# Optimization experiments

Measured on AMD Instinct MI355X. Metric: run time of the kernel, lower is better.

The kernel has to match this reference:

```python
import jax, jax.numpy as jnp
import numpy as np

B, N, P, D = 32, 8, 6, 96
E, H, I, K, NL = 128, 8, 64, 32, 2
L = N * D  # transformer sequence length = 768
OUT = 128
EPS = 1e-5


def _layernorm(x, s, b):
    m = jnp.mean(x, axis=-1, keepdims=True)
    v = jnp.mean((x - m) ** 2, axis=-1, keepdims=True)
    return (x - m) / jnp.sqrt(v + EPS) * s + b


def _pos_encoding(length, d_model):
    pos = jnp.arange(length, dtype=jnp.float32)[:, None]
    div = jnp.exp(jnp.arange(0, d_model, 2, dtype=jnp.float32) * (-jnp.log(10000.0) / d_model))
    ang = pos * div  # [L, E/2]
    return jnp.stack([jnp.sin(ang), jnp.cos(ang)], axis=-1).reshape(length, d_model)


def setup_inputs() -> dict:
    key = jax.random.key(0)
    ks = jax.random.split(key, 20)
    s = 0.02
    return {
        "x": jax.random.normal(ks[0], (B, N, P, D), jnp.float32),
        "prototypes": jax.random.normal(ks[1], (D, K, P), jnp.float32),
        "emb_w": jax.random.normal(ks[2], (E, P), jnp.float32) * s,
        "emb_b": jnp.zeros((E,), jnp.float32),
        "proj_w": jax.random.normal(ks[3], (E, P), jnp.float32) * s,
        "proj_b": jnp.zeros((E,), jnp.float32),
        "in_proj_w": jax.random.normal(ks[4], (NL, 3 * E, E), jnp.float32) * s,
        "in_proj_b": jnp.zeros((NL, 3 * E), jnp.float32),
        "out_proj_w": jax.random.normal(ks[5], (NL, E, E), jnp.float32) * s,
        "out_proj_b": jnp.zeros((NL, E), jnp.float32),
        "ln1_s": jnp.ones((NL, E), jnp.float32),
        "ln1_b": jnp.zeros((NL, E), jnp.float32),
        "ffn_w1": jax.random.normal(ks[6], (NL, I, E), jnp.float32) * s,
        "ffn_b1": jnp.zeros((NL, I), jnp.float32),
        "ffn_w2": jax.random.normal(ks[7], (NL, E, I), jnp.float32) * s,
        "ffn_b2": jnp.zeros((NL, E), jnp.float32),
        "ln2_s": jnp.ones((NL, E), jnp.float32),
        "ln2_b": jnp.zeros((NL, E), jnp.float32),
        "out_w": jax.random.normal(ks[8], (OUT, L * E), jnp.float32) * s,
        "out_b": jnp.zeros((OUT,), jnp.float32),
    }


def reference(x, prototypes, emb_w, emb_b, proj_w, proj_b,
              in_proj_w, in_proj_b, out_proj_w, out_proj_b,
              ln1_s, ln1_b, ffn_w1, ffn_b1, ffn_w2, ffn_b2,
              ln2_s, ln2_b, out_w, out_b):
    # Faithful to torch .view: raw row-major reinterpretation [B,N,P,D] -> [B*N*D, P]
    x_flat = x.reshape(B * N * D, P)
    x_normed = x_flat / jnp.maximum(jnp.linalg.norm(x_flat, axis=1, keepdims=True), 1e-12)
    x_norm = x_normed.reshape(B, N, D, P)
    p_normed = prototypes / jnp.maximum(jnp.linalg.norm(prototypes, axis=2, keepdims=True), 1e-12)

    # Vectorized per-dim cosine-sim argmax + gather (replaces the Python loop over D)
    sim = jnp.einsum('bndp,dkp->bndk', x_norm, p_normed)  # [B,N,D,K]
    best_idx = jnp.argmax(sim, axis=3)                    # [B,N,D]
    d_idx = jnp.arange(D)[None, None, :]
    selected = p_normed[d_idx, best_idx]                  # [B,N,D,P]

    input_embed = (x_flat @ emb_w.T + emb_b).reshape(B, N, D, E)
    proto_embed = (selected.reshape(B * N * D, P) @ proj_w.T + proj_b).reshape(B, N, D, E)
    seq = (input_embed + proto_embed).reshape(B, L, E)
    seq = seq + _pos_encoding(L, E)[None]

    scale = 1.0 / jnp.sqrt(jnp.float32(E // H))
    for l in range(NL):
        qkv = seq @ in_proj_w[l].T + in_proj_b[l]          # [B,L,3E]
        q, k, v = jnp.split(qkv, 3, axis=-1)
        q = q.reshape(B, L, H, E // H)
        k = k.reshape(B, L, H, E // H)
        v = v.reshape(B, L, H, E // H)
        logits = jnp.einsum('blhd,bmhd->bhlm', q, k) * scale
        attn = jax.nn.softmax(logits, axis=-1)
        ctx = jnp.einsum('bhlm,bmhd->blhd', attn, v).reshape(B, L, E)
        attn_out = ctx @ out_proj_w[l].T + out_proj_b[l]
        seq = _layernorm(seq + attn_out, ln1_s[l], ln1_b[l])
        h = jax.nn.elu(seq @ ffn_w1[l].T + ffn_b1[l])
        ffn_out = h @ ffn_w2[l].T + ffn_b2[l]
        seq = _layernorm(seq + ffn_out, ln2_s[l], ln2_b[l])

    z = seq.reshape(B, L * E)
    return z @ out_w.T + out_b
```

## Files before the change

### kernel.cpp

```cpp
#include <hip/hip_runtime.h>
#include <hip/hip_bf16.h>
#include <math.h>

typedef unsigned short ushort_t;
typedef unsigned int uint_t;

#define BB 32
#define PP 6
#define DD 96
#define EE 128
#define HH 8
#define II 64
#define KK 32
#define LSEQ 768
#define ROWS (BB * LSEQ)
#define OUTN 128
#define KOUT (LSEQ * EE)

using bf16x8 = __attribute__((ext_vector_type(8))) short;
using bf16x4 = __attribute__((ext_vector_type(4))) short;
using f32x4  = __attribute__((ext_vector_type(4))) float;
using u32x4  = __attribute__((ext_vector_type(4))) uint_t;

__device__ __forceinline__ ushort_t f2b(float f) {
    __hip_bfloat16 h = __float2bfloat16(f);
    return *reinterpret_cast<ushort_t*>(&h);
}
__device__ __forceinline__ uint_t permpack(float hi, float lo) {
    return __builtin_amdgcn_perm(__builtin_bit_cast(uint_t, hi),
                                 __builtin_bit_cast(uint_t, lo), 0x07060302u);
}

__global__ void cast_all_kernel(
    const float* __restrict__ s0, int n0, const float* __restrict__ s1, int n1,
    const float* __restrict__ s2, int n2, const float* __restrict__ s3, int n3,
    ushort_t* __restrict__ d0, ushort_t* __restrict__ d1,
    ushort_t* __restrict__ d2, ushort_t* __restrict__ d3,
    float* __restrict__ peT)
{
    int i = blockIdx.x * 256 + threadIdx.x;
    if (i < n0) { d0[i] = f2b(s0[i]); return; }
    i -= n0;
    if (i < n1) { d1[i] = f2b(s1[i]); return; }
    i -= n1;
    if (i < n2) { d2[i] = f2b(s2[i]); return; }
    i -= n2;
    if (i < n3) { d3[i] = f2b(s3[i]); return; }
    i -= n3;
    const int lpos = i >> 7, tt = i & 127;
    const float twoj = (float)((tt >> 1) * 2);
    const float div = __expf(twoj * (-9.210340371976184f / 128.0f));
    const float ang = (float)lpos * div;
    peT[i] = (tt & 1) ? __cosf(ang) : __sinf(ang);
}

__global__ __launch_bounds__(128) void embed_kernel(
    const float* __restrict__ x, const float* __restrict__ prot,
    const float* __restrict__ emb_w, const float* __restrict__ emb_b,
    const float* __restrict__ proj_w, const float* __restrict__ proj_b,
    const float* __restrict__ peT,
    float* __restrict__ seq, ushort_t* __restrict__ seq_bf)
{
    const int r = blockIdx.x;
    const int t = threadIdx.x;
    __shared__ float xrow[PP];
    __shared__ float sel[PP];

    if (t < PP) xrow[t] = x[r * PP + t];
    __syncthreads();

    float nx = 0.f;
    #pragma unroll
    for (int p = 0; p < PP; ++p) nx += xrow[p] * xrow[p];
    const float xinv = 1.f / fmaxf(sqrtf(nx), 1e-12f);

    const int d = r % DD;
    if (t < KK) {
        const float* pr = prot + (d * KK + t) * PP;
        float pp[PP];
        float np2 = 0.f;
        #pragma unroll
        for (int p = 0; p < PP; ++p) { pp[p] = pr[p]; np2 += pp[p] * pp[p]; }
        const float pinv = 1.f / fmaxf(sqrtf(np2), 1e-12f);
        float dot = 0.f;
        #pragma unroll
        for (int p = 0; p < PP; ++p) dot += xrow[p] * pp[p];
        float sim = dot * xinv * pinv;
        int k = t;
        #pragma unroll
        for (int off = 16; off; off >>= 1) {
            float osim = __shfl_down(sim, off);
            int   ok   = __shfl_down(k, off);
            if (osim > sim || (osim == sim && ok < k)) { sim = osim; k = ok; }
        }
        k = __shfl(k, 0);
        if (t == k) {
            #pragma unroll
            for (int p = 0; p < PP; ++p) sel[p] = pp[p] * pinv;
        }
    }
    __syncthreads();

    float acc = emb_b[t] + proj_b[t];
    #pragma unroll
    for (int p = 0; p < PP; ++p) acc = fmaf(xrow[p], emb_w[t * PP + p], acc);
    #pragma unroll
    for (int p = 0; p < PP; ++p) acc = fmaf(sel[p], proj_w[t * PP + p], acc);

    const int lpos = r % LSEQ;
    const float v = acc + peT[lpos * EE + t];
    seq[(size_t)r * EE + t] = v;
    seq_bf[(size_t)r * EE + t] = f2b(v);
}

__global__ __launch_bounds__(256) void gemm_qkv(
    const ushort_t* __restrict__ A, const ushort_t* __restrict__ W,
    const float* __restrict__ bias,
    ushort_t* __restrict__ q_bf, ushort_t* __restrict__ k2,
    ushort_t* __restrict__ v2)
{
    __shared__ ushort_t Ws[64 * 136];
    const int t = threadIdx.x;
    const int wave = t >> 6, lane = t & 63;
    const int quad = lane >> 4, l16 = lane & 15;
    const int m0 = blockIdx.y * 128, n0 = blockIdx.x * 64;

    for (int c = t; c < 64 * 16; c += 256) {
        int row = c >> 4, col = c & 15;
        *(bf16x8*)&Ws[row * 136 + col * 8] =
            *(const bf16x8*)&W[(size_t)(n0 + row) * 128 + col * 8];
    }
    __syncthreads();

    f32x4 acc[2][4];
    #pragma unroll
    for (int s = 0; s < 2; ++s)
        #pragma unroll
        for (int nt = 0; nt < 4; ++nt)
            acc[s][nt] = (f32x4){0.f, 0.f, 0.f, 0.f};

    const ushort_t* a0p = A + (size_t)(m0 + wave * 32 + l16) * 128 + quad * 8;
    const ushort_t* a1p = a0p + (size_t)16 * 128;
    const ushort_t* wp  = &Ws[l16 * 136 + quad * 8];

    #pragma unroll
    for (int k0 = 0; k0 < 128; k0 += 32) {
        bf16x8 a0 = *(const bf16x8*)(a0p + k0);
        bf16x8 a1 = *(const bf16x8*)(a1p + k0);
        #pragma unroll
        for (int nt = 0; nt < 4; ++nt) {
            bf16x8 wf = *(const bf16x8*)(wp + nt * 16 * 136 + k0);
            acc[0][nt] = __builtin_amdgcn_mfma_f32_16x16x32_bf16(wf, a0, acc[0][nt], 0, 0, 0);
            acc[1][nt] = __builtin_amdgcn_mfma_f32_16x16x32_bf16(wf, a1, acc[1][nt], 0, 0, 0);
        }
    }

    const int b = blockIdx.y / 6;
    #pragma unroll
    for (int s = 0; s < 2; ++s) {
        const int m = m0 + wave * 32 + s * 16 + l16;
        const int l = m - b * LSEQ;
        const int c4 = l >> 4, r16 = l & 15;
        #pragma unroll
        for (int nt = 0; nt < 4; ++nt) {
            const int nb = n0 + nt * 16 + quad * 4;
            float4 b4 = *(const float4*)&bias[nb];
            float v[4];
            #pragma unroll
            for (int r = 0; r < 4; ++r)
                v[r] = acc[s][nt][r] + ((const float*)&b4)[r];

            if (n0 < 128) {
                #pragma unroll
                for (int r = 0; r < 4; ++r) v[r] *= 0.36067376022224085f;
                uint2 w2;
                w2.x = permpack(v[1], v[0]);
                w2.y = permpack(v[3], v[2]);
                *(uint2*)&q_bf[(size_t)m * EE + nb] = w2;
            } else if (n0 < 256) {
                const int h = ((n0 - 128) >> 4) + nt;
                uint2 w2;
                w2.x = permpack(v[1], v[0]);
                w2.y = permpack(v[3], v[2]);
                *(uint2*)&k2[((((size_t)(b * HH + h)) * 48 + c4) * 4 + quad) * 64 + r16 * 4] = w2;
            } else {
                const int h = ((n0 - 256) >> 4) + nt;
                const size_t vbase = (((size_t)(b * HH + h)) * 48 + c4) * 16;
                #pragma unroll
                for (int r = 0; r < 4; ++r)
                    v2[(vbase + quad * 4 + r) * 16 + r16] = f2b(v[r]);
            }
        }
    }
}

__global__ __launch_bounds__(256) void attention_mfma(
    const ushort_t* __restrict__ q_bf, const ushort_t* __restrict__ k2,
    const ushort_t* __restrict__ v2, ushort_t* __restrict__ ctx)
{
    const int bh = blockIdx.x;
    const int b = bh & 31, h = bh >> 5;
    const int qb = blockIdx.y;
    const int t = threadIdx.x;
    const int wave = t >> 6, lane = t & 63;
    const int quad = lane >> 4, l16 = lane & 15;
    const int hoff = h * 16;

    bf16x4 qf[2];
    #pragma unroll
    for (int s = 0; s < 2; ++s) {
        int row = b * LSEQ + qb * 128 + wave * 32 + s * 16 + l16;
        qf[s] = *(const bf16x4*)&q_bf[(size_t)row * EE + hoff + quad * 4];
    }

    const int bhn = b * HH + h;
    const ushort_t* kp = k2 + (size_t)bhn * 12288 + quad * 64 + l16 * 4;
    const ushort_t* vp = v2 + (size_t)bhn * 12288 + l16 * 16 + quad * 4;

    f32x4 oacc[2], lacc[2];
    oacc[0] = (f32x4){0.f, 0.f, 0.f, 0.f};
    oacc[1] = (f32x4){0.f, 0.f, 0.f, 0.f};
    lacc[0] = (f32x4){0.f, 0.f, 0.f, 0.f};
    lacc[1] = (f32x4){0.f, 0.f, 0.f, 0.f};
    const f32x4 zero4 = (f32x4){0.f, 0.f, 0.f, 0.f};
    bf16x4 ones4;
    #pragma unroll
    for (int j = 0; j < 4; ++j) ones4[j] = (short)0x3F80;

    bf16x4 kA = *(const bf16x4*)(kp);
    bf16x4 vA = *(const bf16x4*)(vp);
    bf16x4 kB = *(const bf16x4*)(kp + 256);
    bf16x4 vB = *(const bf16x4*)(vp + 256);

    for (int c4 = 0; c4 < 48; ++c4) {
        const int c4n = c4 < 46 ? c4 + 2 : 0;
        bf16x4 kC = *(const bf16x4*)(kp + c4n * 256);
        bf16x4 vC = *(const bf16x4*)(vp + c4n * 256);

        #pragma unroll
        for (int s = 0; s < 2; ++s) {
            f32x4 sv = __builtin_amdgcn_mfma_f32_16x16x16bf16_1k(kA, qf[s], zero4, 0, 0, 0);
            float e0 = __builtin_amdgcn_exp2f(sv[0]);
            float e1 = __builtin_amdgcn_exp2f(sv[1]);
            float e2 = __builtin_amdgcn_exp2f(sv[2]);
            float e3 = __builtin_amdgcn_exp2f(sv[3]);
            uint2 pu;
            pu.x = permpack(e1, e0);
            pu.y = permpack(e3, e2);
            bf16x4 pf = __builtin_bit_cast(bf16x4, pu);
            oacc[s] = __builtin_amdgcn_mfma_f32_16x16x16bf16_1k(vA, pf, oacc[s], 0, 0, 0);
            lacc[s] = __builtin_amdgcn_mfma_f32_16x16x16bf16_1k(ones4, pf, lacc[s], 0, 0, 0);
        }
        kA = kB; vA = vB; kB = kC; vB = vC;
    }

    #pragma unroll
    for (int s = 0; s < 2; ++s) {
        const float inv = 1.f / lacc[s][0];
        const int q = qb * 128 + wave * 32 + s * 16 + l16;
        uint2 w2;
        w2.x = permpack(oacc[s][1] * inv, oacc[s][0] * inv);
        w2.y = permpack(oacc[s][3] * inv, oacc[s][2] * inv);
        *(uint2*)&ctx[((size_t)(b * LSEQ + q)) * EE + hoff + quad * 4] = w2;
    }
}

__global__ __launch_bounds__(256) void gemm_ln_direct(
    const ushort_t* __restrict__ A, const ushort_t* __restrict__ W,
    const float* __restrict__ bias,
    const float* __restrict__ gamma, const float* __restrict__ beta,
    float* __restrict__ seq, ushort_t* __restrict__ seq_bf, int K)
{
    __shared__ ushort_t Ws[128 * 136];
    const int t = threadIdx.x;
    const int wave = t >> 6, lane = t & 63;
    const int quad = lane >> 4, l16 = lane & 15;
    const int m0 = blockIdx.x * 64;
    const int kp = K + 8;
    const int ak8 = K >> 3;

    for (int c = t; c < 128 * ak8; c += 256) {
        int row = c / ak8, col = c - row * ak8;
        *(bf16x8*)&Ws[row * kp + col * 8] =
            *(const bf16x8*)&W[(size_t)row * K + col * 8];
    }
    __syncthreads();

    f32x4 acc[8];
    #pragma unroll
    for (int nt = 0; nt < 8; ++nt) acc[nt] = (f32x4){0.f, 0.f, 0.f, 0.f};

    const int m = m0 + wave * 16 + l16;
    const ushort_t* ap = A + (size_t)m * K + quad * 8;
    const ushort_t* wp = &Ws[l16 * kp + quad * 8];

    for (int k0 = 0; k0 < K; k0 += 32) {
        bf16x8 a = *(const bf16x8*)(ap + k0);
        #pragma unroll
        for (int nt = 0; nt < 8; ++nt) {
            bf16x8 wf = *(const bf16x8*)(wp + nt * 16 * kp + k0);
            acc[nt] = __builtin_amdgcn_mfma_f32_16x16x32_bf16(wf, a, acc[nt], 0, 0, 0);
        }
    }

    float v[8][4];
    float s = 0.f;
    #pragma unroll
    for (int nt = 0; nt < 8; ++nt) {
        const int nb = nt * 16 + quad * 4;
        float4 b4 = *(const float4*)&bias[nb];
        float4 r4 = *(const float4*)&seq[(size_t)m * EE + nb];
        #pragma unroll
        for (int r = 0; r < 4; ++r) {
            v[nt][r] = acc[nt][r] + ((const float*)&b4)[r] + ((const float*)&r4)[r];
            s += v[nt][r];
        }
    }
    s += __shfl_xor(s, 16);
    s += __shfl_xor(s, 32);
    const float mean = s * (1.f / 128.f);
    float s2 = 0.f;
    #pragma unroll
    for (int nt = 0; nt < 8; ++nt)
        #pragma unroll
        for (int r = 0; r < 4; ++r) {
            float d = v[nt][r] - mean;
            s2 += d * d;
        }
    s2 += __shfl_xor(s2, 16);
    s2 += __shfl_xor(s2, 32);
    const float rstd = 1.f / sqrtf(s2 * (1.f / 128.f) + 1e-5f);

    #pragma unroll
    for (int nt = 0; nt < 8; ++nt) {
        const int nb = nt * 16 + quad * 4;
        float4 g4 = *(const float4*)&gamma[nb];
        float4 be4 = *(const float4*)&beta[nb];
        float y[4];
        #pragma unroll
        for (int r = 0; r < 4; ++r)
            y[r] = (v[nt][r] - mean) * rstd * ((const float*)&g4)[r] + ((const float*)&be4)[r];
        float4 f4 = {y[0], y[1], y[2], y[3]};
        *(float4*)&seq[(size_t)m * EE + nb] = f4;
        uint2 w2;
        w2.x = permpack(y[1], y[0]);
        w2.y = permpack(y[3], y[2]);
        *(uint2*)&seq_bf[(size_t)m * EE + nb] = w2;
    }
}

__global__ __launch_bounds__(256) void ffn_fused(
    const ushort_t* __restrict__ seq_bf_in, const ushort_t* __restrict__ W1,
    const float* __restrict__ b1, const ushort_t* __restrict__ W2,
    const float* __restrict__ b2,
    const float* __restrict__ gamma, const float* __restrict__ beta,
    float* __restrict__ seq, ushort_t* __restrict__ seq_bf)
{
    __shared__ ushort_t W1s[64 * 136];
    __shared__ ushort_t W2s[128 * 72];
    __shared__ ushort_t Hs[64 * 72];
    const int t = threadIdx.x;
    const int wave = t >> 6, lane = t & 63;
    const int quad = lane >> 4, l16 = lane & 15;
    const int m0 = blockIdx.x * 64;

    for (int c = t; c < 64 * 16; c += 256) {
        int row = c >> 4, col = c & 15;
        *(bf16x8*)&W1s[row * 136 + col * 8] =
            *(const bf16x8*)&W1[(size_t)row * 128 + col * 8];
    }
    for (int c = t; c < 128 * 8; c += 256) {
        int row = c >> 3, col = c & 7;
        *(bf16x8*)&W2s[row * 72 + col * 8] =
            *(const bf16x8*)&W2[(size_t)row * 64 + col * 8];
    }
    __syncthreads();

    const int lrow = wave * 16 + l16;
    const int m = m0 + lrow;
    f32x4 acc1[4];
    #pragma unroll
    for (int nt = 0; nt < 4; ++nt) acc1[nt] = (f32x4){0.f, 0.f, 0.f, 0.f};

    const ushort_t* ap = seq_bf_in + (size_t)m * EE + quad * 8;
    const ushort_t* w1p = &W1s[l16 * 136 + quad * 8];
    for (int k0 = 0; k0 < 128; k0 += 32) {
        bf16x8 a = *(const bf16x8*)(ap + k0);
        #pragma unroll
        for (int nt = 0; nt < 4; ++nt) {
            bf16x8 wf = *(const bf16x8*)(w1p + nt * 16 * 136 + k0);
            acc1[nt] = __builtin_amdgcn_mfma_f32_16x16x32_bf16(wf, a, acc1[nt], 0, 0, 0);
        }
    }
    #pragma unroll
    for (int nt = 0; nt < 4; ++nt) {
        const int ib = nt * 16 + quad * 4;
        float4 b4 = *(const float4*)&b1[ib];
        float hv[4];
        #pragma unroll
        for (int r = 0; r < 4; ++r) {
            float u = acc1[nt][r] + ((const float*)&b4)[r];
            hv[r] = u > 0.f ? u : expm1f(u);
        }
        uint2 w2;
        w2.x = permpack(hv[1], hv[0]);
        w2.y = permpack(hv[3], hv[2]);
        *(uint2*)&Hs[lrow * 72 + ib] = w2;
    }

    f32x4 acc2[8];
    #pragma unroll
    for (int nt = 0; nt < 8; ++nt) acc2[nt] = (f32x4){0.f, 0.f, 0.f, 0.f};
    const ushort_t* hp = &Hs[lrow * 72 + quad * 8];
    const ushort_t* w2p = &W2s[l16 * 72 + quad * 8];
    #pragma unroll
    for (int k0 = 0; k0 < 64; k0 += 32) {
        bf16x8 hf = *(const bf16x8*)(hp + k0);
        #pragma unroll
        for (int nt = 0; nt < 8; ++nt) {
            bf16x8 wf = *(const bf16x8*)(w2p + nt * 16 * 72 + k0);
            acc2[nt] = __builtin_amdgcn_mfma_f32_16x16x32_bf16(wf, hf, acc2[nt], 0, 0, 0);
        }
    }

    float v[8][4];
    float s = 0.f;
    #pragma unroll
    for (int nt = 0; nt < 8; ++nt) {
        const int nb = nt * 16 + quad * 4;
        float4 b4 = *(const float4*)&b2[nb];
        float4 r4 = *(const float4*)&seq[(size_t)m * EE + nb];
        #pragma unroll
        for (int r = 0; r < 4; ++r) {
            v[nt][r] = acc2[nt][r] + ((const float*)&b4)[r] + ((const float*)&r4)[r];
            s += v[nt][r];
        }
    }
    s += __shfl_xor(s, 16);
    s += __shfl_xor(s, 32);
    const float mean = s * (1.f / 128.f);
    float s2 = 0.f;
    #pragma unroll
    for (int nt = 0; nt < 8; ++nt)
        #pragma unroll
        for (int r = 0; r < 4; ++r) {
            float d = v[nt][r] - mean;
            s2 += d * d;
        }
    s2 += __shfl_xor(s2, 16);
    s2 += __shfl_xor(s2, 32);
    const float rstd = 1.f / sqrtf(s2 * (1.f / 128.f) + 1e-5f);

    #pragma unroll
    for (int nt = 0; nt < 8; ++nt) {
        const int nb = nt * 16 + quad * 4;
        float4 g4 = *(const float4*)&gamma[nb];
        float4 be4 = *(const float4*)&beta[nb];
        float y[4];
        #pragma unroll
        for (int r = 0; r < 4; ++r)
            y[r] = (v[nt][r] - mean) * rstd * ((const float*)&g4)[r] + ((const float*)&be4)[r];
        float4 f4 = {y[0], y[1], y[2], y[3]};
        *(float4*)&seq[(size_t)m * EE + nb] = f4;
        uint2 w2;
        w2.x = permpack(y[1], y[0]);
        w2.y = permpack(y[3], y[2]);
        *(uint2*)&seq_bf[(size_t)m * EE + nb] = w2;
    }
}

#define PKC 192
#define PNBLK (KOUT / PKC)
__global__ __launch_bounds__(256) void out_gemm3(
    const ushort_t* __restrict__ seqbf, const float* __restrict__ out_w,
    float* __restrict__ part)
{
    const int t = threadIdx.x;
    const int wave = t >> 6, lane = t & 63;
    const int quad = lane >> 4, l16 = lane & 15;
    const size_t k0 = (size_t)blockIdx.x * PKC;
    const int n0 = wave * 32;

    f32x4 acc[2][2];
    #pragma unroll
    for (int mt = 0; mt < 2; ++mt)
        #pragma unroll
        for (int nt = 0; nt < 2; ++nt)
            acc[mt][nt] = (f32x4){0.f, 0.f, 0.f, 0.f};

    const ushort_t* a0p = seqbf + (size_t)l16 * KOUT + k0 + quad * 8;
    const ushort_t* a1p = a0p + (size_t)16 * KOUT;
    const float* w0p = out_w + (size_t)(n0 + l16) * KOUT + k0 + quad * 8;
    const float* w1p = w0p + (size_t)16 * KOUT;

    #pragma unroll
    for (int ks = 0; ks < PKC; ks += 32) {
        bf16x8 a0 = *(const bf16x8*)(a0p + ks);
        bf16x8 a1 = *(const bf16x8*)(a1p + ks);
        float4 wa0 = *(const float4*)(w0p + ks);
        float4 wa1 = *(const float4*)(w0p + ks + 4);
        float4 wb0 = *(const float4*)(w1p + ks);
        float4 wb1 = *(const float4*)(w1p + ks + 4);
        u32x4 b0, b1;
        b0[0] = permpack(wa0.y, wa0.x); b0[1] = permpack(wa0.w, wa0.z);
        b0[2] = permpack(wa1.y, wa1.x); b0[3] = permpack(wa1.w, wa1.z);
        b1[0] = permpack(wb0.y, wb0.x); b1[1] = permpack(wb0.w, wb0.z);
        b1[2] = permpack(wb1.y, wb1.x); b1[3] = permpack(wb1.w, wb1.z);
        bf16x8 bf0 = __builtin_bit_cast(bf16x8, b0);
        bf16x8 bf1 = __builtin_bit_cast(bf16x8, b1);
        acc[0][0] = __builtin_amdgcn_mfma_f32_16x16x32_bf16(a0, bf0, acc[0][0], 0, 0, 0);
        acc[1][0] = __builtin_amdgcn_mfma_f32_16x16x32_bf16(a1, bf0, acc[1][0], 0, 0, 0);
        acc[0][1] = __builtin_amdgcn_mfma_f32_16x16x32_bf16(a0, bf1, acc[0][1], 0, 0, 0);
        acc[1][1] = __builtin_amdgcn_mfma_f32_16x16x32_bf16(a1, bf1, acc[1][1], 0, 0, 0);
    }

    float* pb = part + (size_t)blockIdx.x * (32 * 128);
    #pragma unroll
    for (int mt = 0; mt < 2; ++mt)
        #pragma unroll
        for (int nt = 0; nt < 2; ++nt)
            #pragma unroll
            for (int r = 0; r < 4; ++r)
                pb[(mt * 16 + quad * 4 + r) * 128 + n0 + nt * 16 + l16] = acc[mt][nt][r];
}

__global__ __launch_bounds__(256) void out_reduce1(
    const float* __restrict__ part, float* __restrict__ part2)
{
    const int g = blockIdx.x & 15, rr = blockIdx.x >> 4;
    const int i = g * 256 + threadIdx.x;
    const float* p = part + (size_t)rr * 64 * 4096 + i;
    float s0 = 0.f, s1 = 0.f, s2 = 0.f, s3 = 0.f;
    for (int blk = 0; blk < 64; blk += 4) {
        s0 += p[(size_t)blk * 4096];
        s1 += p[(size_t)(blk + 1) * 4096];
        s2 += p[(size_t)(blk + 2) * 4096];
        s3 += p[(size_t)(blk + 3) * 4096];
    }
    part2[rr * 4096 + i] = (s0 + s1) + (s2 + s3);
}

__global__ __launch_bounds__(256) void out_reduce2(
    const float* __restrict__ part2, const float* __restrict__ out_b,
    float* __restrict__ out)
{
    const int i = blockIdx.x * 256 + threadIdx.x;
    float s = 0.f;
    #pragma unroll
    for (int rr = 0; rr < 8; ++rr) s += part2[rr * 4096 + i];
    out[i] = out_b[i & (OUTN - 1)] + s;
}

extern "C" void kernel_launch(void* const* d_in, const int* in_sizes, int n_in,
                              void* d_out, int out_size, void* d_ws, size_t ws_size,
                              hipStream_t stream)
{
    const float* x          = (const float*)d_in[0];
    const float* prototypes = (const float*)d_in[1];
    const float* emb_w      = (const float*)d_in[2];
    const float* emb_b      = (const float*)d_in[3];
    const float* proj_w     = (const float*)d_in[4];
    const float* proj_b     = (const float*)d_in[5];
    const float* in_proj_w  = (const float*)d_in[6];
    const float* in_proj_b  = (const float*)d_in[7];
    const float* out_proj_w = (const float*)d_in[8];
    const float* out_proj_b = (const float*)d_in[9];
    const float* ln1_s      = (const float*)d_in[10];
    const float* ln1_b      = (const float*)d_in[11];
    const float* ffn_w1     = (const float*)d_in[12];
    const float* ffn_b1     = (const float*)d_in[13];
    const float* ffn_w2     = (const float*)d_in[14];
    const float* ffn_b2     = (const float*)d_in[15];
    const float* ln2_s      = (const float*)d_in[16];
    const float* ln2_b      = (const float*)d_in[17];
    const float* out_w      = (const float*)d_in[18];
    const float* out_b      = (const float*)d_in[19];
    float* out = (float*)d_out;
    char* base = (char*)d_ws;

    float*    seq    = (float*)base;
    float*    tmp    = (float*)(base + 12582912);
    ushort_t* seq_bf = (ushort_t*)(base + 25165824);
    ushort_t* q_bf   = (ushort_t*)(base + 31457280);
    ushort_t* k2     = (ushort_t*)(base + 37748736);
    ushort_t* v2     = (ushort_t*)(base + 44040192);
    ushort_t* ctx_bf = (ushort_t*)(base + 50331648);
    ushort_t* w_bf   = (ushort_t*)(base + 56623104);
    float*    part   = tmp;
    float*    part2  = (float*)(base + 12582912 + 8388608);
    float*    peT    = (float*)(base + 12582912 + 9437184);
    (void)ws_size;

    ushort_t* w_in  = w_bf;
    ushort_t* w_out = w_bf + 98304;
    ushort_t* w_f1  = w_bf + 131072;
    ushort_t* w_f2  = w_bf + 147456;

    cast_all_kernel<<<1024, 256, 0, stream>>>(
        in_proj_w, 98304, out_proj_w, 32768, ffn_w1, 16384, ffn_w2, 16384,
        w_in, w_out, w_f1, w_f2, peT);

    embed_kernel<<<ROWS, 128, 0, stream>>>(x, prototypes, emb_w, emb_b,
                                           proj_w, proj_b, peT, seq, seq_bf);

    for (int l = 0; l < 2; ++l) {
        gemm_qkv<<<dim3(6, 192), 256, 0, stream>>>(
            seq_bf, w_in + (size_t)l * 49152, in_proj_b + l * 384,
            q_bf, k2, v2);
        attention_mfma<<<dim3(BB * HH, 6), 256, 0, stream>>>(q_bf, k2, v2, ctx_bf);
        gemm_ln_direct<<<ROWS / 64, 256, 0, stream>>>(
            ctx_bf, w_out + (size_t)l * 16384, out_proj_b + l * 128,
            ln1_s + l * EE, ln1_b + l * EE, seq, seq_bf, 128);
        ffn_fused<<<ROWS / 64, 256, 0, stream>>>(
            seq_bf, w_f1 + (size_t)l * 8192, ffn_b1 + l * II,
            w_f2 + (size_t)l * 8192, ffn_b2 + l * EE,
            ln2_s + l * EE, ln2_b + l * EE, seq, seq_bf);
    }

    out_gemm3<<<PNBLK, 256, 0, stream>>>(seq_bf, out_w, part);
    out_reduce1<<<128, 256, 0, stream>>>(part, part2);
    out_reduce2<<<BB * OUTN / 256, 256, 0, stream>>>(part2, out_b, out);
}
```

Baseline: 297.0 us.

## Fuse out-proj+LN1 with FFN+LN2, deepen attention prefetch, merge output reductions

Merges the out-projection/LayerNorm kernel with the FFN/LayerNorm kernel so the LN1 result stays in registers and shared memory instead of going through global memory. The final layer also skips writing the fp32 residual. The attention loop now prefetches four K/V chunks ahead with manual unrolling instead of two. The output GEMM uses a larger K chunk per block, and its two-stage reduction becomes one kernel. The cost is more shared memory per block in the fused kernel, which may lower occupancy, plus fewer, longer output GEMM blocks.

```diff
diff --git a/kernel.cpp b/kernel.cpp
--- a/kernel.cpp
+++ b/kernel.cpp
@@ -194,6 +194,27 @@
     }
 }
 
+__device__ __forceinline__ void attn_step(
+    bf16x4 kf, bf16x4 vf, const bf16x4 (&qf)[2],
+    f32x4 (&oacc)[2], f32x4 (&lacc)[2], bf16x4 ones4)
+{
+    const f32x4 zero4 = (f32x4){0.f, 0.f, 0.f, 0.f};
+    #pragma unroll
+    for (int s = 0; s < 2; ++s) {
+        f32x4 sv = __builtin_amdgcn_mfma_f32_16x16x16bf16_1k(kf, qf[s], zero4, 0, 0, 0);
+        float e0 = __builtin_amdgcn_exp2f(sv[0]);
+        float e1 = __builtin_amdgcn_exp2f(sv[1]);
+        float e2 = __builtin_amdgcn_exp2f(sv[2]);
+        float e3 = __builtin_amdgcn_exp2f(sv[3]);
+        uint2 pu;
+        pu.x = permpack(e1, e0);
+        pu.y = permpack(e3, e2);
+        bf16x4 pf = __builtin_bit_cast(bf16x4, pu);
+        oacc[s] = __builtin_amdgcn_mfma_f32_16x16x16bf16_1k(vf, pf, oacc[s], 0, 0, 0);
+        lacc[s] = __builtin_amdgcn_mfma_f32_16x16x16bf16_1k(ones4, pf, lacc[s], 0, 0, 0);
+    }
+}
+
 __global__ __launch_bounds__(256) void attention_mfma(
     const ushort_t* __restrict__ q_bf, const ushort_t* __restrict__ k2,
     const ushort_t* __restrict__ v2, ushort_t* __restrict__ ctx)
@@ -222,36 +243,32 @@
     oacc[1] = (f32x4){0.f, 0.f, 0.f, 0.f};
     lacc[0] = (f32x4){0.f, 0.f, 0.f, 0.f};
     lacc[1] = (f32x4){0.f, 0.f, 0.f, 0.f};
-    const f32x4 zero4 = (f32x4){0.f, 0.f, 0.f, 0.f};
     bf16x4 ones4;
     #pragma unroll
     for (int j = 0; j < 4; ++j) ones4[j] = (short)0x3F80;
 
-    bf16x4 kA = *(const bf16x4*)(kp);
-    bf16x4 vA = *(const bf16x4*)(vp);
-    bf16x4 kB = *(const bf16x4*)(kp + 256);
-    bf16x4 vB = *(const bf16x4*)(vp + 256);
-
-    for (int c4 = 0; c4 < 48; ++c4) {
-        const int c4n = c4 < 46 ? c4 + 2 : 0;
-        bf16x4 kC = *(const bf16x4*)(kp + c4n * 256);
-        bf16x4 vC = *(const bf16x4*)(vp + c4n * 256);
-
-        #pragma unroll
-        for (int s = 0; s < 2; ++s) {
-            f32x4 sv = __builtin_amdgcn_mfma_f32_16x16x16bf16_1k(kA, qf[s], zero4, 0, 0, 0);
-            float e0 = __builtin_amdgcn_exp2f(sv[0]);
-            float e1 = __builtin_amdgcn_exp2f(sv[1]);
-            float e2 = __builtin_amdgcn_exp2f(sv[2]);
-            float e3 = __builtin_amdgcn_exp2f(sv[3]);
-            uint2 pu;
-            pu.x = permpack(e1, e0);
-            pu.y = permpack(e3, e2);
-            bf16x4 pf = __builtin_bit_cast(bf16x4, pu);
-            oacc[s] = __builtin_amdgcn_mfma_f32_16x16x16bf16_1k(vA, pf, oacc[s], 0, 0, 0);
-            lacc[s] = __builtin_amdgcn_mfma_f32_16x16x16bf16_1k(ones4, pf, lacc[s], 0, 0, 0);
-        }
-        kA = kB; vA = vB; kB = kC; vB = vC;
+    bf16x4 kb0 = *(const bf16x4*)(kp);
+    bf16x4 vb0 = *(const bf16x4*)(vp);
+    bf16x4 kb1 = *(const bf16x4*)(kp + 256);
+    bf16x4 vb1 = *(const bf16x4*)(vp + 256);
+    bf16x4 kb2 = *(const bf16x4*)(kp + 512);
+    bf16x4 vb2 = *(const bf16x4*)(vp + 512);
+    bf16x4 kb3 = *(const bf16x4*)(kp + 768);
+    bf16x4 vb3 = *(const bf16x4*)(vp + 768);
+
+    for (int c0 = 0; c0 < 48; c0 += 4) {
+        attn_step(kb0, vb0, qf, oacc, lacc, ones4);
+        { int n = c0 + 4; n = n >= 48 ? n - 48 : n;
+          kb0 = *(const bf16x4*)(kp + n * 256); vb0 = *(const bf16x4*)(vp + n * 256); }
+        attn_step(kb1, vb1, qf, oacc, lacc, ones4);
+        { int n = c0 + 5; n = n >= 48 ? n - 48 : n;
+          kb1 = *(const bf16x4*)(kp + n * 256); vb1 = *(const bf16x4*)(vp + n * 256); }
+        attn_step(kb2, vb2, qf, oacc, lacc, ones4);
+        { int n = c0 + 6; n = n >= 48 ? n - 48 : n;
+          kb2 = *(const bf16x4*)(kp + n * 256); vb2 = *(const bf16x4*)(vp + n * 256); }
+        attn_step(kb3, vb3, qf, oacc, lacc, ones4);
+        { int n = c0 + 7; n = n >= 48 ? n - 48 : n;
+          kb3 = *(const bf16x4*)(kp + n * 256); vb3 = *(const bf16x4*)(vp + n * 256); }
     }
 
     #pragma unroll
@@ -265,131 +282,120 @@
     }
 }
 
-__global__ __launch_bounds__(256) void gemm_ln_direct(
-    const ushort_t* __restrict__ A, const ushort_t* __restrict__ W,
-    const float* __restrict__ bias,
-    const float* __restrict__ gamma, const float* __restrict__ beta,
-    float* __restrict__ seq, ushort_t* __restrict__ seq_bf, int K)
-{
-    __shared__ ushort_t Ws[128 * 136];
+#define W1OFF 0
+#define W2OFF 8704
+#define YOFF  17920
+#define HOFF  26624
+__global__ __launch_bounds__(256) void gemm_ln_ffn(
+    const ushort_t* __restrict__ ctx_bf, const ushort_t* __restrict__ Wout,
+    const float* __restrict__ bout,
+    const float* __restrict__ g1, const float* __restrict__ be1,
+    const ushort_t* __restrict__ W1, const float* __restrict__ b1,
+    const ushort_t* __restrict__ W2, const float* __restrict__ b2,
+    const float* __restrict__ g2, const float* __restrict__ be2,
+    float* __restrict__ seq, ushort_t* __restrict__ seq_bf, int write_f32)
+{
+    __shared__ ushort_t S[31232];
     const int t = threadIdx.x;
     const int wave = t >> 6, lane = t & 63;
     const int quad = lane >> 4, l16 = lane & 15;
     const int m0 = blockIdx.x * 64;
-    const int kp = K + 8;
-    const int ak8 = K >> 3;
-
-    for (int c = t; c < 128 * ak8; c += 256) {
-        int row = c / ak8, col = c - row * ak8;
-        *(bf16x8*)&Ws[row * kp + col * 8] =
-            *(const bf16x8*)&W[(size_t)row * K + col * 8];
+    const int lrow = wave * 16 + l16;
+    const int m = m0 + lrow;
+
+    for (int c = t; c < 128 * 16; c += 256) {
+        int row = c >> 4, col = c & 15;
+        *(bf16x8*)&S[row * 136 + col * 8] =
+            *(const bf16x8*)&Wout[(size_t)row * 128 + col * 8];
     }
     __syncthreads();
 
     f32x4 acc[8];
     #pragma unroll
     for (int nt = 0; nt < 8; ++nt) acc[nt] = (f32x4){0.f, 0.f, 0.f, 0.f};
-
-    const int m = m0 + wave * 16 + l16;
-    const ushort_t* ap = A + (size_t)m * K + quad * 8;
-    const ushort_t* wp = &Ws[l16 * kp + quad * 8];
-
-    for (int k0 = 0; k0 < K; k0 += 32) {
-        bf16x8 a = *(const bf16x8*)(ap + k0);
-        #pragma unroll
-        for (int nt = 0; nt < 8; ++nt) {
-            bf16x8 wf = *(const bf16x8*)(wp + nt * 16 * kp + k0);
-            acc[nt] = __builtin_amdgcn_mfma_f32_16x16x32_bf16(wf, a, acc[nt], 0, 0, 0);
-        }
-    }
-
-    float v[8][4];
+    {
+        const ushort_t* ap = ctx_bf + (size_t)m * EE + quad * 8;
+        const ushort_t* wp = &S[l16 * 136 + quad * 8];
+        #pragma unroll
+        for (int k0 = 0; k0 < 128; k0 += 32) {
+            bf16x8 a = *(const bf16x8*)(ap + k0);
+            #pragma unroll
+            for (int nt = 0; nt < 8; ++nt) {
+                bf16x8 wf = *(const bf16x8*)(wp + nt * 16 * 136 + k0);
+                acc[nt] = __builtin_amdgcn_mfma_f32_16x16x32_bf16(wf, a, acc[nt], 0, 0, 0);
+            }
+        }
+    }
+    __syncthreads();
+
+    for (int c = t; c < 64 * 16; c += 256) {
+        int row = c >> 4, col = c & 15;
+        *(bf16x8*)&S[W1OFF + row * 136 + col * 8] =
+            *(const bf16x8*)&W1[(size_t)row * 128 + col * 8];
+    }
+    for (int c = t; c < 128 * 8; c += 256) {
+        int row = c >> 3, col = c & 7;
+        *(bf16x8*)&S[W2OFF + row * 72 + col * 8] =
+            *(const bf16x8*)&W2[(size_t)row * 64 + col * 8];
+    }
+
+    float y[8][4];
     float s = 0.f;
     #pragma unroll
     for (int nt = 0; nt < 8; ++nt) {
         const int nb = nt * 16 + quad * 4;
-        float4 b4 = *(const float4*)&bias[nb];
+        float4 b4 = *(const float4*)&bout[nb];
         float4 r4 = *(const float4*)&seq[(size_t)m * EE + nb];
         #pragma unroll
         for (int r = 0; r < 4; ++r) {
-            v[nt][r] = acc[nt][r] + ((const float*)&b4)[r] + ((const float*)&r4)[r];
-            s += v[nt][r];
+            y[nt][r] = acc[nt][r] + ((const float*)&b4)[r] + ((const float*)&r4)[r];
+            s += y[nt][r];
         }
     }
     s += __shfl_xor(s, 16);
     s += __shfl_xor(s, 32);
-    const float mean = s * (1.f / 128.f);
+    float mean = s * (1.f / 128.f);
     float s2 = 0.f;
     #pragma unroll
     for (int nt = 0; nt < 8; ++nt)
         #pragma unroll
         for (int r = 0; r < 4; ++r) {
-            float d = v[nt][r] - mean;
+            float d = y[nt][r] - mean;
             s2 += d * d;
         }
     s2 += __shfl_xor(s2, 16);
     s2 += __shfl_xor(s2, 32);
-    const float rstd = 1.f / sqrtf(s2 * (1.f / 128.f) + 1e-5f);
+    float rstd = 1.f / sqrtf(s2 * (1.f / 128.f) + 1e-5f);
 
     #pragma unroll
     for (int nt = 0; nt < 8; ++nt) {
         const int nb = nt * 16 + quad * 4;
-        float4 g4 = *(const float4*)&gamma[nb];
-        float4 be4 = *(const float4*)&beta[nb];
-        float y[4];
+        float4 g4 = *(const float4*)&g1[nb];
+        float4 be4 = *(const float4*)&be1[nb];
         #pragma unroll
         for (int r = 0; r < 4; ++r)
-            y[r] = (v[nt][r] - mean) * rstd * ((const float*)&g4)[r] + ((const float*)&be4)[r];
-        float4 f4 = {y[0], y[1], y[2], y[3]};
-        *(float4*)&seq[(size_t)m * EE + nb] = f4;
+            y[nt][r] = (y[nt][r] - mean) * rstd * ((const float*)&g4)[r] + ((const float*)&be4)[r];
         uint2 w2;
-        w2.x = permpack(y[1], y[0]);
-        w2.y = permpack(y[3], y[2]);
-        *(uint2*)&seq_bf[(size_t)m * EE + nb] = w2;
-    }
-}
-
-__global__ __launch_bounds__(256) void ffn_fused(
-    const ushort_t* __restrict__ seq_bf_in, const ushort_t* __restrict__ W1,
-    const float* __restrict__ b1, const ushort_t* __restrict__ W2,
-    const float* __restrict__ b2,
-    const float* __restrict__ gamma, const float* __restrict__ beta,
-    float* __restrict__ seq, ushort_t* __restrict__ seq_bf)
-{
-    __shared__ ushort_t W1s[64 * 136];
-    __shared__ ushort_t W2s[128 * 72];
-    __shared__ ushort_t Hs[64 * 72];
-    const int t = threadIdx.x;
-    const int wave = t >> 6, lane = t & 63;
-    const int quad = lane >> 4, l16 = lane & 15;
-    const int m0 = blockIdx.x * 64;
-
-    for (int c = t; c < 64 * 16; c += 256) {
-        int row = c >> 4, col = c & 15;
-        *(bf16x8*)&W1s[row * 136 + col * 8] =
-            *(const bf16x8*)&W1[(size_t)row * 128 + col * 8];
-    }
-    for (int c = t; c < 128 * 8; c += 256) {
-        int row = c >> 3, col = c & 7;
-        *(bf16x8*)&W2s[row * 72 + col * 8] =
-            *(const bf16x8*)&W2[(size_t)row * 64 + col * 8];
+        w2.x = permpack(y[nt][1], y[nt][0]);
+        w2.y = permpack(y[nt][3], y[nt][2]);
+        *(uint2*)&S[YOFF + lrow * 136 + nb] = w2;
     }
     __syncthreads();
 
-    const int lrow = wave * 16 + l16;
-    const int m = m0 + lrow;
     f32x4 acc1[4];
     #pragma unroll
     for (int nt = 0; nt < 4; ++nt) acc1[nt] = (f32x4){0.f, 0.f, 0.f, 0.f};
-
-    const ushort_t* ap = seq_bf_in + (size_t)m * EE + quad * 8;
-    const ushort_t* w1p = &W1s[l16 * 136 + quad * 8];
-    for (int k0 = 0; k0 < 128; k0 += 32) {
-        bf16x8 a = *(const bf16x8*)(ap + k0);
-        #pragma unroll
-        for (int nt = 0; nt < 4; ++nt) {
-            bf16x8 wf = *(const bf16x8*)(w1p + nt * 16 * 136 + k0);
-            acc1[nt] = __builtin_amdgcn_mfma_f32_16x16x32_bf16(wf, a, acc1[nt], 0, 0, 0);
+    {
+        const ushort_t* ap1 = &S[YOFF + lrow * 136 + quad * 8];
+        const ushort_t* w1p = &S[W1OFF + l16 * 136 + quad * 8];
+        #pragma unroll
+        for (int k0 = 0; k0 < 128; k0 += 32) {
+            bf16x8 a = *(const bf16x8*)(ap1 + k0);
+            #pragma unroll
+            for (int nt = 0; nt < 4; ++nt) {
+                bf16x8 wf = *(const bf16x8*)(w1p + nt * 16 * 136 + k0);
+                acc1[nt] = __builtin_amdgcn_mfma_f32_16x16x32_bf16(wf, a, acc1[nt], 0, 0, 0);
+            }
         }
     }
     #pragma unroll
@@ -405,41 +411,42 @@
         uint2 w2;
         w2.x = permpack(hv[1], hv[0]);
         w2.y = permpack(hv[3], hv[2]);
-        *(uint2*)&Hs[lrow * 72 + ib] = w2;
+        *(uint2*)&S[HOFF + lrow * 72 + ib] = w2;
     }
 
     f32x4 acc2[8];
     #pragma unroll
     for (int nt = 0; nt < 8; ++nt) acc2[nt] = (f32x4){0.f, 0.f, 0.f, 0.f};
-    const ushort_t* hp = &Hs[lrow * 72 + quad * 8];
-    const ushort_t* w2p = &W2s[l16 * 72 + quad * 8];
-    #pragma unroll
-    for (int k0 = 0; k0 < 64; k0 += 32) {
-        bf16x8 hf = *(const bf16x8*)(hp + k0);
-        #pragma unroll
-        for (int nt = 0; nt < 8; ++nt) {
-            bf16x8 wf = *(const bf16x8*)(w2p + nt * 16 * 72 + k0);
-            acc2[nt] = __builtin_amdgcn_mfma_f32_16x16x32_bf16(wf, hf, acc2[nt], 0, 0, 0);
+    {
+        const ushort_t* hp  = &S[HOFF + lrow * 72 + quad * 8];
+        const ushort_t* w2p = &S[W2OFF + l16 * 72 + quad * 8];
+        #pragma unroll
+        for (int k0 = 0; k0 < 64; k0 += 32) {
+            bf16x8 hf = *(const bf16x8*)(hp + k0);
+            #pragma unroll
+            for (int nt = 0; nt < 8; ++nt) {
+                bf16x8 wf = *(const bf16x8*)(w2p + nt * 16 * 72 + k0);
+                acc2[nt] = __builtin_amdgcn_mfma_f32_16x16x32_bf16(wf, hf, acc2[nt], 0, 0, 0);
+            }
         }
     }
 
     float v[8][4];
-    float s = 0.f;
+    s = 0.f;
     #pragma unroll
     for (int nt = 0; nt < 8; ++nt) {
         const int nb = nt * 16 + quad * 4;
         float4 b4 = *(const float4*)&b2[nb];
-        float4 r4 = *(const float4*)&seq[(size_t)m * EE + nb];
         #pragma unroll
         for (int r = 0; r < 4; ++r) {
-            v[nt][r] = acc2[nt][r] + ((const float*)&b4)[r] + ((const float*)&r4)[r];
+            v[nt][r] = acc2[nt][r] + ((const float*)&b4)[r] + y[nt][r];
             s += v[nt][r];
         }
     }
     s += __shfl_xor(s, 16);
     s += __shfl_xor(s, 32);
-    const float mean = s * (1.f / 128.f);
-    float s2 = 0.f;
+    mean = s * (1.f / 128.f);
+    s2 = 0.f;
     #pragma unroll
     for (int nt = 0; nt < 8; ++nt)
         #pragma unroll
@@ -449,27 +456,29 @@
         }
     s2 += __shfl_xor(s2, 16);
     s2 += __shfl_xor(s2, 32);
-    const float rstd = 1.f / sqrtf(s2 * (1.f / 128.f) + 1e-5f);
+    rstd = 1.f / sqrtf(s2 * (1.f / 128.f) + 1e-5f);
 
     #pragma unroll
     for (int nt = 0; nt < 8; ++nt) {
         const int nb = nt * 16 + quad * 4;
-        float4 g4 = *(const float4*)&gamma[nb];
-        float4 be4 = *(const float4*)&beta[nb];
-        float y[4];
+        float4 g4 = *(const float4*)&g2[nb];
+        float4 be4 = *(const float4*)&be2[nb];
+        float o[4];
         #pragma unroll
         for (int r = 0; r < 4; ++r)
-            y[r] = (v[nt][r] - mean) * rstd * ((const float*)&g4)[r] + ((const float*)&be4)[r];
-        float4 f4 = {y[0], y[1], y[2], y[3]};
-        *(float4*)&seq[(size_t)m * EE + nb] = f4;
+            o[r] = (v[nt][r] - mean) * rstd * ((const float*)&g4)[r] + ((const float*)&be4)[r];
+        if (write_f32) {
+            float4 f4 = {o[0], o[1], o[2], o[3]};
+            *(float4*)&seq[(size_t)m * EE + nb] = f4;
+        }
         uint2 w2;
-        w2.x = permpack(y[1], y[0]);
-        w2.y = permpack(y[3], y[2]);
+        w2.x = permpack(o[1], o[0]);
+        w2.y = permpack(o[3], o[2]);
         *(uint2*)&seq_bf[(size_t)m * EE + nb] = w2;
     }
 }
 
-#define PKC 192
+#define PKC 384
 #define PNBLK (KOUT / PKC)
 __global__ __launch_bounds__(256) void out_gemm3(
     const ushort_t* __restrict__ seqbf, const float* __restrict__ out_w,
@@ -493,7 +502,6 @@
     const float* w0p = out_w + (size_t)(n0 + l16) * KOUT + k0 + quad * 8;
     const float* w1p = w0p + (size_t)16 * KOUT;
 
-    #pragma unroll
     for (int ks = 0; ks < PKC; ks += 32) {
         bf16x8 a0 = *(const bf16x8*)(a0p + ks);
         bf16x8 a1 = *(const bf16x8*)(a1p + ks);
@@ -524,31 +532,20 @@
                 pb[(mt * 16 + quad * 4 + r) * 128 + n0 + nt * 16 + l16] = acc[mt][nt][r];
 }
 
-__global__ __launch_bounds__(256) void out_reduce1(
-    const float* __restrict__ part, float* __restrict__ part2)
-{
-    const int g = blockIdx.x & 15, rr = blockIdx.x >> 4;
-    const int i = g * 256 + threadIdx.x;
-    const float* p = part + (size_t)rr * 64 * 4096 + i;
+__global__ __launch_bounds__(256) void out_reduce(
+    const float* __restrict__ part, const float* __restrict__ out_b,
+    float* __restrict__ out)
+{
+    const int i = blockIdx.x * 256 + threadIdx.x;
+    const float* p = part + i;
     float s0 = 0.f, s1 = 0.f, s2 = 0.f, s3 = 0.f;
-    for (int blk = 0; blk < 64; blk += 4) {
+    for (int blk = 0; blk < PNBLK; blk += 4) {
         s0 += p[(size_t)blk * 4096];
         s1 += p[(size_t)(blk + 1) * 4096];
         s2 += p[(size_t)(blk + 2) * 4096];
         s3 += p[(size_t)(blk + 3) * 4096];
     }
-    part2[rr * 4096 + i] = (s0 + s1) + (s2 + s3);
-}
-
-__global__ __launch_bounds__(256) void out_reduce2(
-    const float* __restrict__ part2, const float* __restrict__ out_b,
-    float* __restrict__ out)
-{
-    const int i = blockIdx.x * 256 + threadIdx.x;
-    float s = 0.f;
-    #pragma unroll
-    for (int rr = 0; rr < 8; ++rr) s += part2[rr * 4096 + i];
-    out[i] = out_b[i & (OUTN - 1)] + s;
+    out[i] = out_b[i & (OUTN - 1)] + ((s0 + s1) + (s2 + s3));
 }
 
 extern "C" void kernel_launch(void* const* d_in, const int* in_sizes, int n_in,
@@ -587,7 +584,6 @@
     ushort_t* ctx_bf = (ushort_t*)(base + 50331648);
     ushort_t* w_bf   = (ushort_t*)(base + 56623104);
     float*    part   = tmp;
-    float*    part2  = (float*)(base + 12582912 + 8388608);
     float*    peT    = (float*)(base + 12582912 + 9437184);
     (void)ws_size;
 
@@ -608,16 +604,15 @@
             seq_bf, w_in + (size_t)l * 49152, in_proj_b + l * 384,
             q_bf, k2, v2);
         attention_mfma<<<dim3(BB * HH, 6), 256, 0, stream>>>(q_bf, k2, v2, ctx_bf);
-        gemm_ln_direct<<<ROWS / 64, 256, 0, stream>>>(
+        gemm_ln_ffn<<<ROWS / 64, 256, 0, stream>>>(
             ctx_bf, w_out + (size_t)l * 16384, out_proj_b + l * 128,
-            ln1_s + l * EE, ln1_b + l * EE, seq, seq_bf, 128);
-        ffn_fused<<<ROWS / 64, 256, 0, stream>>>(
-            seq_bf, w_f1 + (size_t)l * 8192, ffn_b1 + l * II,
+            ln1_s + l * EE, ln1_b + l * EE,
+            w_f1 + (size_t)l * 8192, ffn_b1 + l * II,
             w_f2 + (size_t)l * 8192, ffn_b2 + l * EE,
-            ln2_s + l * EE, ln2_b + l * EE, seq, seq_bf);
+            ln2_s + l * EE, ln2_b + l * EE,
+            seq, seq_bf, l == 0 ? 1 : 0);
     }
 
     out_gemm3<<<PNBLK, 256, 0, stream>>>(seq_bf, out_w, part);
-    out_reduce1<<<128, 256, 0, stream>>>(part, part2);
-    out_reduce2<<<BB * OUTN / 256, 256, 0, stream>>>(part2, out_b, out);
-}
+    out_reduce<<<BB * OUTN / 256, 256, 0, stream>>>(part, out_b, out);
+}
```

New measurement: 282.4 us. -4.9%, faster.
